# Performance work log

Measured on AMD Instinct MI355X. Metric: run time of the kernel, lower is better.

## Reference

```python
import jax, jax.numpy as jnp
import numpy as np
from jax import lax

B, W_LEN, V, E, C, K, L = 8, 1000, 50000, 100, 50, 3, 18000


def setup_inputs() -> dict:
    key = jax.random.key(0)
    ks = jax.random.split(key, 7)
    return {
        "x": jax.random.randint(ks[0], (B, W_LEN), 0, V),
        "W_embed": jax.random.normal(ks[1], (V, E), dtype=jnp.float32) * 0.1,
        "conv_w": jax.random.normal(ks[2], (C, E, K), dtype=jnp.float32) * 0.08,
        "conv_b": jax.random.normal(ks[3], (C,), dtype=jnp.float32) * 0.01,
        "u_w": jax.random.normal(ks[4], (L, C), dtype=jnp.float32) * 0.1,
        "out_w": jax.random.normal(ks[5], (L, C), dtype=jnp.float32) * 0.1,
        "out_b": jax.random.normal(ks[6], (L,), dtype=jnp.float32) * 0.01,
    }


def reference(x, W_embed, conv_w, conv_b, u_w, out_w, out_b):
    # embedding lookup: (B, W, E)
    emb = W_embed[x]
    # conv1d over sequence, 'same' padding: (B, C, W)
    emb_ncw = jnp.transpose(emb, (0, 2, 1))
    H = lax.conv_general_dilated(
        emb_ncw, conv_w, window_strides=(1,), padding=[(K // 2, K // 2)],
        dimension_numbers=("NCH", "OIH", "NCH"))
    H = jnp.tanh(H + conv_b[None, :, None])
    H = jnp.transpose(H, (0, 2, 1))  # (B, W, C)
    # label-wise attention scores: (B, L, W), softmax over seq
    scores = jnp.einsum("lc,bwc->blw", u_w, H)
    attns = jax.nn.softmax(scores, axis=2)
    # attention-pooled reps: (B, L, C)
    m = jnp.einsum("blw,bwc->blc", attns, H)
    # per-label weighted dot product + bias, sigmoid: (B, L)
    out = jax.nn.sigmoid(jnp.sum(out_w[None] * m, axis=2) + out_b[None])
    return out
```

## Files before the change

### kernel.cpp

```cpp
#include <hip/hip_runtime.h>
#include <hip/hip_bf16.h>
#include <cmath>

#define AS1 __attribute__((address_space(1)))
#define AS3 __attribute__((address_space(3)))

#define B_ 8
#define W_LEN_ 1000
#define WP 1024
#define E_ 100
#define C_ 50
#define CPAD 64
#define HP 72
#define K_ 3
#define L_ 18000
#define TL 64
#define NLBLK ((L_ + TL - 1) / TL)
#define CWT 16
#define NSLOT (K_ * (E_ / 4))

typedef __attribute__((ext_vector_type(8))) short bf16x8;
typedef __attribute__((ext_vector_type(4))) short bf16x4;
typedef __attribute__((ext_vector_type(4))) float f32x4;

static __device__ __forceinline__ void gl_lds16(const void* g, void* l) {
    __builtin_amdgcn_global_load_lds((const AS1 unsigned*)g, (AS3 unsigned*)l, 16, 0, 0);
}
static __device__ __forceinline__ float bf2f(short s) {
    return __uint_as_float(((unsigned)(unsigned short)s) << 16);
}

__global__ __launch_bounds__(256) void prep_w(
    const float* __restrict__ conv_w, bf16x4* __restrict__ cwTs)
{
    int idx = blockIdx.x * blockDim.x + threadIdx.x;
    if (idx >= NSLOT * C_) return;
    int slot = idx / C_;
    int c    = idx % C_;
    int k = slot / (E_ / 4);
    int i = slot % (E_ / 4);
    bf16x4 v;
    #pragma unroll
    for (int q = 0; q < 4; q++) {
        __hip_bfloat16 h = __float2bfloat16(conv_w[((size_t)c * E_ + 4 * i + q) * K_ + k]);
        v[q] = *reinterpret_cast<short*>(&h);
    }
    cwTs[idx] = v;
}

__global__ __launch_bounds__(256) void prep_uo(
    const float* __restrict__ u_w, const float* __restrict__ out_w,
    __hip_bfloat16* __restrict__ UO)
{
    int tid = blockIdx.x * blockDim.x + threadIdx.x;
    if (tid >= 2 * L_ * CPAD) return;
    int c = tid & (CPAD - 1);
    int l = (tid >> 6) % L_;
    int m = tid / (L_ * CPAD);
    const float* src = m ? out_w : u_w;
    float v = (c < C_) ? src[(size_t)l * C_ + c] : 0.f;
    UO[tid] = __float2bfloat16(v);
}

__global__ __launch_bounds__(256) void conv_kernel(
    const int* __restrict__ x,
    const float* __restrict__ W_embed,
    const bf16x4* __restrict__ cwTs,
    const float* __restrict__ conv_b,
    __hip_bfloat16* __restrict__ H)
{
    __shared__ float4 emb_s[(CWT + 2) * (E_ / 4)];
    __shared__ bf16x4 wS[NSLOT * C_];

    const int b  = blockIdx.y;
    const int w0 = blockIdx.x * CWT;
    const int tid = threadIdx.x;

    for (int i = tid; i < NSLOT * C_; i += 256) wS[i] = cwTs[i];

    for (int i = tid; i < (CWT + 2) * (E_ / 4); i += 256) {
        int row = i / (E_ / 4);
        int e4  = i % (E_ / 4);
        int ws  = w0 - 1 + row;
        float4 v = make_float4(0.f, 0.f, 0.f, 0.f);
        if ((unsigned)ws < (unsigned)W_LEN_)
            v = ((const float4*)(W_embed + (size_t)x[b * W_LEN_ + ws] * E_))[e4];
        emb_s[i] = v;
    }
    __syncthreads();

    const int c  = tid & 63;
    const int wq = tid >> 6;
    const int cc = (c < C_) ? c : 0;

    f32x4 acc[4];
    const float bias = conv_b[cc];
    #pragma unroll
    for (int j = 0; j < 4; j++) acc[j] = (f32x4){bias, 0.f, 0.f, 0.f};

    const float4* eb = &emb_s[wq * 4 * (E_ / 4)];

    #pragma unroll 5
    for (int i = 0; i < E_ / 4; i++) {
        bf16x4 kb0 = wS[i * C_ + cc];
        bf16x4 kb1 = wS[(25 + i) * C_ + cc];
        bf16x4 kb2 = wS[(50 + i) * C_ + cc];
        float4 k0 = make_float4(bf2f(kb0[0]), bf2f(kb0[1]), bf2f(kb0[2]), bf2f(kb0[3]));
        float4 k1 = make_float4(bf2f(kb1[0]), bf2f(kb1[1]), bf2f(kb1[2]), bf2f(kb1[3]));
        float4 k2 = make_float4(bf2f(kb2[0]), bf2f(kb2[1]), bf2f(kb2[2]), bf2f(kb2[3]));
        float4 e0 = eb[i],       e1 = eb[25 + i],  e2 = eb[50 + i];
        float4 e3 = eb[75 + i],  e4 = eb[100 + i], e5 = eb[125 + i];
        acc[0].x += e0.x*k0.x + e1.x*k1.x + e2.x*k2.x;
        acc[0].y += e0.y*k0.y + e1.y*k1.y + e2.y*k2.y;
        acc[0].z += e0.z*k0.z + e1.z*k1.z + e2.z*k2.z;
        acc[0].w += e0.w*k0.w + e1.w*k1.w + e2.w*k2.w;
        acc[1].x += e1.x*k0.x + e2.x*k1.x + e3.x*k2.x;
        acc[1].y += e1.y*k0.y + e2.y*k1.y + e3.y*k2.y;
        acc[1].z += e1.z*k0.z + e2.z*k1.z + e3.z*k2.z;
        acc[1].w += e1.w*k0.w + e2.w*k1.w + e3.w*k2.w;
        acc[2].x += e2.x*k0.x + e3.x*k1.x + e4.x*k2.x;
        acc[2].y += e2.y*k0.y + e3.y*k1.y + e4.y*k2.y;
        acc[2].z += e2.z*k0.z + e3.z*k1.z + e4.z*k2.z;
        acc[2].w += e2.w*k0.w + e3.w*k1.w + e4.w*k2.w;
        acc[3].x += e3.x*k0.x + e4.x*k1.x + e5.x*k2.x;
        acc[3].y += e3.y*k0.y + e4.y*k1.y + e5.y*k2.y;
        acc[3].z += e3.z*k0.z + e4.z*k1.z + e5.z*k2.z;
        acc[3].w += e3.w*k0.w + e4.w*k1.w + e5.w*k2.w;
    }

    #pragma unroll
    for (int j = 0; j < 4; j++) {
        int w = w0 + wq * 4 + j;
        float v = 0.f;
        if (c < C_ && w < W_LEN_)
            v = tanhf((acc[j].x + acc[j].z) + (acc[j].y + acc[j].w));
        __hip_bfloat16* row = H + ((size_t)b * WP + w) * HP;
        row[c] = __float2bfloat16(v);
        if (c < HP - 64) row[64 + c] = __float2bfloat16(0.f);
    }
}

__global__ __launch_bounds__(256) void attn_kernel(
    const __hip_bfloat16* __restrict__ H,
    const __hip_bfloat16* __restrict__ UO,
    const float* __restrict__ out_b,
    float* __restrict__ out)
{
    __shared__ __hip_bfloat16 Hs[2][64 * HP];
    __shared__ float2 red[2][TL];

    const int b  = blockIdx.y;
    const int l0 = blockIdx.x * TL;
    const int tid  = threadIdx.x;
    const int lane = tid & 63;
    const int wid  = tid >> 6;
    const int mi = wid & 1, ni = wid >> 1;
    const int col = lane & 15, quad = lane >> 4;

    bf16x8 Uf[2][2], Of[2][2];
    #pragma unroll
    for (int mt = 0; mt < 2; mt++) {
        int l = l0 + mi * 32 + mt * 16 + col;
        if (l >= L_) l = L_ - 1;
        const __hip_bfloat16* up = UO + (size_t)l * CPAD + quad * 8;
        const __hip_bfloat16* op = up + (size_t)L_ * CPAD;
        #pragma unroll
        for (int st = 0; st < 2; st++) {
            Uf[mt][st] = *(const bf16x8*)(up + st * 32);
            Of[mt][st] = *(const bf16x8*)(op + st * 32);
        }
    }

    f32x4 lsum[2] = {{0.f,0.f,0.f,0.f},{0.f,0.f,0.f,0.f}};
    f32x4 num [2] = {{0.f,0.f,0.f,0.f},{0.f,0.f,0.f,0.f}};
    const f32x4 zero = {0.f, 0.f, 0.f, 0.f};

    const __hip_bfloat16* Hb = H + (size_t)b * WP * HP;

    {
        const char* g = (const char*)Hb;
        char* l = (char*)&Hs[0][0];
        gl_lds16(g + tid * 16,         l + tid * 16);
        gl_lds16(g + (tid + 256) * 16, l + (tid + 256) * 16);
        if (tid < 64)
            gl_lds16(g + (tid + 512) * 16, l + (tid + 512) * 16);
    }

    #pragma unroll 1
    for (int wt = 0; wt < WP; wt += 64) {
        const int cur = (wt >> 6) & 1;
        __syncthreads();

        if (wt + 64 < WP) {
            const char* g = (const char*)(Hb + (size_t)(wt + 64) * HP);
            char* l = (char*)&Hs[cur ^ 1][0];
            gl_lds16(g + tid * 16,         l + tid * 16);
            gl_lds16(g + (tid + 256) * 16, l + (tid + 256) * 16);
            if (tid < 64)
                gl_lds16(g + (tid + 512) * 16, l + (tid + 512) * 16);
        }

        bf16x8 Bc[2][2];
        #pragma unroll
        for (int nt = 0; nt < 2; nt++)
            #pragma unroll
            for (int st = 0; st < 2; st++)
                Bc[nt][st] = *(const bf16x8*)(&Hs[cur][(ni * 32 + nt * 16 + col) * HP
                                                       + quad * 8 + st * 32]);

        #pragma unroll
        for (int nt = 0; nt < 2; nt++) {
            #pragma unroll
            for (int mt = 0; mt < 2; mt++) {
                f32x4 S = __builtin_amdgcn_mfma_f32_16x16x32_bf16(Uf[mt][0], Bc[nt][0], zero, 0, 0, 0);
                S       = __builtin_amdgcn_mfma_f32_16x16x32_bf16(Uf[mt][1], Bc[nt][1], S,    0, 0, 0);
                f32x4 T = __builtin_amdgcn_mfma_f32_16x16x32_bf16(Of[mt][0], Bc[nt][0], zero, 0, 0, 0);
                T       = __builtin_amdgcn_mfma_f32_16x16x32_bf16(Of[mt][1], Bc[nt][1], T,    0, 0, 0);
                #pragma unroll
                for (int r = 0; r < 4; r++) {
                    float p = __expf(S[r]);
                    lsum[mt][r] += p;
                    num [mt][r] += p * T[r];
                }
            }
        }
    }

    #pragma unroll
    for (int mt = 0; mt < 2; mt++) {
        #pragma unroll
        for (int r = 0; r < 4; r++) {
            float ls = lsum[mt][r], nm = num[mt][r];
            #pragma unroll
            for (int d = 1; d < 16; d <<= 1) {
                ls += __shfl_xor(ls, d, 64);
                nm += __shfl_xor(nm, d, 64);
            }
            if (col == 0)
                red[ni][mi * 32 + mt * 16 + quad * 4 + r] = make_float2(ls, nm);
        }
    }
    __syncthreads();

    if (tid < TL) {
        int l = l0 + tid;
        if (l < L_) {
            float2 p0 = red[0][tid], p1 = red[1][tid];
            float z = (p0.y + p1.y) / (p0.x + p1.x - (float)(WP - W_LEN_)) + out_b[l];
            out[(size_t)b * L_ + l] = 1.f / (1.f + __expf(-z));
        }
    }
}

extern "C" void kernel_launch(void* const* d_in, const int* in_sizes, int n_in,
                              void* d_out, int out_size, void* d_ws, size_t ws_size,
                              hipStream_t stream) {
    const int*   x       = (const int*)  d_in[0];
    const float* W_embed = (const float*)d_in[1];
    const float* conv_w  = (const float*)d_in[2];
    const float* conv_b  = (const float*)d_in[3];
    const float* u_w     = (const float*)d_in[4];
    const float* out_w   = (const float*)d_in[5];
    const float* out_b   = (const float*)d_in[6];
    float* out = (float*)d_out;

    char* ws = (char*)d_ws;
    __hip_bfloat16* H  = (__hip_bfloat16*)ws;
    __hip_bfloat16* UO = (__hip_bfloat16*)(ws + 1179648);
    bf16x4*       cwTs = (bf16x4*)(ws + 1179648 + 4608000);

    {
        const int total = NSLOT * C_;
        prep_w<<<dim3((total + 255) / 256), 256, 0, stream>>>(conv_w, cwTs);
    }
    {
        const int total = 2 * L_ * CPAD;
        prep_uo<<<dim3((total + 255) / 256), 256, 0, stream>>>(u_w, out_w, UO);
    }
    {
        dim3 grid(WP / CWT, B_);
        conv_kernel<<<grid, 256, 0, stream>>>(x, W_embed, cwTs, conv_b, H);
    }
    {
        dim3 grid(NLBLK, B_);
        attn_kernel<<<grid, 256, 0, stream>>>(H, UO, out_b, out);
    }
}
```

Baseline: 152.9 us.

## Widen attention label tile to 128 and merge prep kernels

Each attention block now handles 128 labels, and each wave owns 32 labels across all 64 sequence positions of a tile. This removes the cross-wave LDS reduction and its barrier, and halves how often each block streams H through LDS. The two prep kernels are merged into one launch to save launch overhead, and the sequence loop is unrolled by 2. The trade-offs are more B-fragment registers per wave and half as many blocks in the grid, which may reduce occupancy.

```diff
diff --git a/kernel.cpp b/kernel.cpp
--- a/kernel.cpp
+++ b/kernel.cpp
@@ -14,7 +14,7 @@
 #define HP 72
 #define K_ 3
 #define L_ 18000
-#define TL 64
+#define TL 128
 #define NLBLK ((L_ + TL - 1) / TL)
 #define CWT 16
 #define NSLOT (K_ * (E_ / 4))
@@ -30,36 +30,33 @@
     return __uint_as_float(((unsigned)(unsigned short)s) << 16);
 }
 
-__global__ __launch_bounds__(256) void prep_w(
-    const float* __restrict__ conv_w, bf16x4* __restrict__ cwTs)
-{
-    int idx = blockIdx.x * blockDim.x + threadIdx.x;
-    if (idx >= NSLOT * C_) return;
-    int slot = idx / C_;
-    int c    = idx % C_;
-    int k = slot / (E_ / 4);
-    int i = slot % (E_ / 4);
-    bf16x4 v;
-    #pragma unroll
-    for (int q = 0; q < 4; q++) {
-        __hip_bfloat16 h = __float2bfloat16(conv_w[((size_t)c * E_ + 4 * i + q) * K_ + k]);
-        v[q] = *reinterpret_cast<short*>(&h);
-    }
-    cwTs[idx] = v;
-}
-
-__global__ __launch_bounds__(256) void prep_uo(
-    const float* __restrict__ u_w, const float* __restrict__ out_w,
-    __hip_bfloat16* __restrict__ UO)
+__global__ __launch_bounds__(256) void prep_all(
+    const float* __restrict__ conv_w, const float* __restrict__ u_w,
+    const float* __restrict__ out_w,
+    bf16x4* __restrict__ cwTs, __hip_bfloat16* __restrict__ UO)
 {
     int tid = blockIdx.x * blockDim.x + threadIdx.x;
-    if (tid >= 2 * L_ * CPAD) return;
-    int c = tid & (CPAD - 1);
-    int l = (tid >> 6) % L_;
-    int m = tid / (L_ * CPAD);
-    const float* src = m ? out_w : u_w;
-    float v = (c < C_) ? src[(size_t)l * C_ + c] : 0.f;
-    UO[tid] = __float2bfloat16(v);
+    if (tid < NSLOT * C_) {
+        int slot = tid / C_;
+        int c    = tid % C_;
+        int k = slot / (E_ / 4);
+        int i = slot % (E_ / 4);
+        bf16x4 v;
+        #pragma unroll
+        for (int q = 0; q < 4; q++) {
+            __hip_bfloat16 h = __float2bfloat16(conv_w[((size_t)c * E_ + 4 * i + q) * K_ + k]);
+            v[q] = *reinterpret_cast<short*>(&h);
+        }
+        cwTs[tid] = v;
+    }
+    if (tid < 2 * L_ * CPAD) {
+        int c = tid & (CPAD - 1);
+        int l = (tid >> 6) % L_;
+        int m = tid / (L_ * CPAD);
+        const float* src = m ? out_w : u_w;
+        float v = (c < C_) ? src[(size_t)l * C_ + c] : 0.f;
+        UO[tid] = __float2bfloat16(v);
+    }
 }
 
 __global__ __launch_bounds__(256) void conv_kernel(
@@ -147,20 +144,18 @@
     float* __restrict__ out)
 {
     __shared__ __hip_bfloat16 Hs[2][64 * HP];
-    __shared__ float2 red[2][TL];
 
     const int b  = blockIdx.y;
     const int l0 = blockIdx.x * TL;
     const int tid  = threadIdx.x;
     const int lane = tid & 63;
     const int wid  = tid >> 6;
-    const int mi = wid & 1, ni = wid >> 1;
     const int col = lane & 15, quad = lane >> 4;
 
     bf16x8 Uf[2][2], Of[2][2];
     #pragma unroll
     for (int mt = 0; mt < 2; mt++) {
-        int l = l0 + mi * 32 + mt * 16 + col;
+        int l = l0 + wid * 32 + mt * 16 + col;
         if (l >= L_) l = L_ - 1;
         const __hip_bfloat16* up = UO + (size_t)l * CPAD + quad * 8;
         const __hip_bfloat16* op = up + (size_t)L_ * CPAD;
@@ -186,7 +181,7 @@
             gl_lds16(g + (tid + 512) * 16, l + (tid + 512) * 16);
     }
 
-    #pragma unroll 1
+    #pragma unroll 2
     for (int wt = 0; wt < WP; wt += 64) {
         const int cur = (wt >> 6) & 1;
         __syncthreads();
@@ -200,16 +195,16 @@
                 gl_lds16(g + (tid + 512) * 16, l + (tid + 512) * 16);
         }
 
-        bf16x8 Bc[2][2];
-        #pragma unroll
-        for (int nt = 0; nt < 2; nt++)
+        bf16x8 Bc[4][2];
+        #pragma unroll
+        for (int nt = 0; nt < 4; nt++)
             #pragma unroll
             for (int st = 0; st < 2; st++)
-                Bc[nt][st] = *(const bf16x8*)(&Hs[cur][(ni * 32 + nt * 16 + col) * HP
+                Bc[nt][st] = *(const bf16x8*)(&Hs[cur][(nt * 16 + col) * HP
                                                        + quad * 8 + st * 32]);
 
         #pragma unroll
-        for (int nt = 0; nt < 2; nt++) {
+        for (int nt = 0; nt < 4; nt++) {
             #pragma unroll
             for (int mt = 0; mt < 2; mt++) {
                 f32x4 S = __builtin_amdgcn_mfma_f32_16x16x32_bf16(Uf[mt][0], Bc[nt][0], zero, 0, 0, 0);
@@ -236,18 +231,13 @@
                 ls += __shfl_xor(ls, d, 64);
                 nm += __shfl_xor(nm, d, 64);
             }
-            if (col == 0)
-                red[ni][mi * 32 + mt * 16 + quad * 4 + r] = make_float2(ls, nm);
-        }
-    }
-    __syncthreads();
-
-    if (tid < TL) {
-        int l = l0 + tid;
-        if (l < L_) {
-            float2 p0 = red[0][tid], p1 = red[1][tid];
-            float z = (p0.y + p1.y) / (p0.x + p1.x - (float)(WP - W_LEN_)) + out_b[l];
-            out[(size_t)b * L_ + l] = 1.f / (1.f + __expf(-z));
+            if (col == 0) {
+                int l = l0 + wid * 32 + mt * 16 + quad * 4 + r;
+                if (l < L_) {
+                    float z = nm / (ls - (float)(WP - W_LEN_)) + out_b[l];
+                    out[(size_t)b * L_ + l] = 1.f / (1.f + __expf(-z));
+                }
+            }
         }
     }
 }
@@ -270,12 +260,8 @@
     bf16x4*       cwTs = (bf16x4*)(ws + 1179648 + 4608000);
 
     {
-        const int total = NSLOT * C_;
-        prep_w<<<dim3((total + 255) / 256), 256, 0, stream>>>(conv_w, cwTs);
-    }
-    {
         const int total = 2 * L_ * CPAD;
-        prep_uo<<<dim3((total + 255) / 256), 256, 0, stream>>>(u_w, out_w, UO);
+        prep_all<<<dim3((total + 255) / 256), 256, 0, stream>>>(conv_w, u_w, out_w, cwTs, UO);
     }
     {
         dim3 grid(WP / CWT, B_);
```

Measured after the change: 155.9 us. About the same (+1.9%).
